# Optimization experiments

Measured on AMD Instinct MI355X. Metric: run time of the kernel, lower is better.

## Reference

```python
import jax, jax.numpy as jnp
import numpy as np

INP = 768      # inp_dim
HID = 768      # head_dim * head_num
H = 8          # head_num
D = 96         # head_dim
UP = 1536      # p_factor * inp_dim
KER = 4        # causal conv kernel size
CAP = 15.0     # gate_soft_cap
EPS = 1e-6
FUSED_OUT = 2 * H + 4 * HID  # 3088: i(8) f(8) o(768) q(768) k(768) v(768)


def _ln(x, g, b):
    mu = jnp.mean(x, axis=-1, keepdims=True)
    var = jnp.mean(jnp.square(x - mu), axis=-1, keepdims=True)
    return (x - mu) * jax.lax.rsqrt(var + EPS) * g + b


def setup_inputs() -> dict:
    key = jax.random.key(0)
    ks = jax.random.split(key, 8)
    s = 0.02
    return {
        "x": jax.random.normal(ks[0], (8, 1024, INP), dtype=jnp.float32),
        "ln1_g": jnp.ones((INP,), jnp.float32),
        "ln1_b": jnp.zeros((INP,), jnp.float32),
        "W_up_l": jax.random.normal(ks[1], (UP, INP), jnp.float32) * s,
        "W_up_r": jax.random.normal(ks[2], (HID, INP), jnp.float32) * s,
        "conv_w": jax.random.normal(ks[3], (KER,), jnp.float32) * 0.5,
        "W_skip": jax.random.normal(ks[4], (HID, UP), jnp.float32) * s,
        "fused_W": jax.random.normal(ks[5], (FUSED_OUT, UP), jnp.float32) * s,
        "fused_b": jnp.zeros((FUSED_OUT,), jnp.float32),
        "ln2_g": jnp.ones((HID,), jnp.float32),
        "ln2_b": jnp.zeros((HID,), jnp.float32),
        "W_down": jax.random.normal(ks[6], (INP, HID), jnp.float32) * s,
    }


def reference(x, ln1_g, ln1_b, W_up_l, W_up_r, conv_w, W_skip,
              fused_W, fused_b, ln2_g, ln2_b, W_down):
    B, S, _ = x.shape
    inv_sqrt_d = 1.0 / np.sqrt(D).astype(np.float32)

    def step(carry, x_row):           # x_row: [B, INP]
        C, n, m = carry               # [B,H,D,D], [B,H,D], [B,H]
        x_n = _ln(x_row, ln1_g, ln1_b)
        xt = x_n @ W_up_l.T           # [B, UP]
        rt = x_n @ W_up_r.T           # [B, HID]
        # causal conv over feature axis (left pad ker-1, 4-tap correlation)
        xp = jnp.pad(xt, ((0, 0), (KER - 1, 0)))
        xc = conv_w[0] * xp[:, 0:UP] + conv_w[1] * xp[:, 1:1 + UP] \
           + conv_w[2] * xp[:, 2:2 + UP] + conv_w[3] * xp[:, 3:3 + UP]
        xc = jax.nn.silu(xc)
        x_skip = xc @ W_skip.T        # [B, HID]
        fused = xc @ fused_W.T + fused_b  # [B, 3088]
        i_t = CAP * jnp.tanh(fused[:, :H] / CAP)                   # [B,H]
        f_t = CAP * jnp.tanh(fused[:, H:2 * H] / CAP)              # [B,H]
        # NOTE: original soft-caps o_gate too ('gate' in name) before sigmoid
        o_t = jax.nn.sigmoid(CAP * jnp.tanh(fused[:, 2 * H:2 * H + HID] / CAP))
        q = fused[:, 2 * H + HID:2 * H + 2 * HID].reshape(B, H, D)
        k = fused[:, 2 * H + 2 * HID:2 * H + 3 * HID].reshape(B, H, D) * inv_sqrt_d
        v = fused[:, 2 * H + 3 * HID:].reshape(B, H, D)
        m_t = jnp.maximum(f_t + m, i_t)
        ie = jnp.exp(i_t - m_t)
        fe = jnp.exp(f_t - m_t + m)
        C_t = fe[:, :, None, None] * C + ie[:, :, None, None] * jnp.einsum('bhd,bhe->bhde', v, k)
        n_t = fe[:, :, None] * n + ie[:, :, None] * k
        h_num = jnp.einsum('bhde,bhe->bhd', C_t, q)
        h_den = jnp.maximum(jnp.sum(n_t * q, axis=-1, keepdims=True), 1.0)
        h = o_t * (h_num / h_den).reshape(B, HID)
        out = _ln(h, ln2_g, ln2_b) @ W_down.T + x_skip
        out = out * jax.nn.silu(rt)
        return (C_t, n_t, m_t), out + x_row

    C0 = jnp.zeros((B, H, D, D), x.dtype)
    n0 = jnp.ones((B, H, D), x.dtype)
    m0 = jnp.zeros((B, H), x.dtype)
    (Cf, nf, mf), ys = jax.lax.scan(step, (C0, n0, m0), jnp.swapaxes(x, 0, 1))
    return jnp.swapaxes(ys, 0, 1), Cf, nf, mf
```

## Files before the change

### kernel.cpp

```cpp
#include <hip/hip_runtime.h>
#include <hip/hip_bf16.h>

#define NH 8
#define NB 8
#define NS 1024
#define NTOK (NB*NS)
#define CAPV 15.0f
#define EPSV 1e-6f
#define NPAD_UP 2304
#define SFW3 3968
#define OQKV_W 3072
#define INV_SQRT_D 0.10206207261596575f
#define YS_ELEMS ((size_t)NTOK * 768)
#define CH 64
#define NCH 16

typedef __attribute__((ext_vector_type(8))) short short8;
typedef __attribute__((ext_vector_type(4))) float f32x4;
typedef __hip_bfloat16 bf16;

__device__ inline float cvt(float v) { return v; }
__device__ inline float cvt(bf16 v) { return __bfloat162float(v); }

__device__ __forceinline__ void gll16(const void* g, void* l) {
  __builtin_amdgcn_global_load_lds(
      (const __attribute__((address_space(1))) void*)g,
      (__attribute__((address_space(3))) void*)l, 16, 0, 0);
}

__global__ void cast_pad_kernel(const float* __restrict__ src, bf16* __restrict__ dst, long n) {
  long i = (long)blockIdx.x * 256 + threadIdx.x;
  if (i < n) dst[i] = __float2bfloat16(src[i]);
}

__global__ void build_wsf2_kernel(const float* __restrict__ Wskip, const float* __restrict__ fusedW,
                                  bf16* __restrict__ dst) {
  int k = blockIdx.x * 256 + threadIdx.x;
  int r = blockIdx.y;
  float v;
  if (r < 768) v = Wskip[(size_t)r * 1536 + k];
  else if (r < 784) v = fusedW[(size_t)(r - 768) * 1536 + k];
  else if (r < 832) v = 0.f;
  else if (r < 3904) v = fusedW[(size_t)(r - 816) * 1536 + k];
  else v = 0.f;
  dst[(size_t)r * 1536 + k] = __float2bfloat16(v);
}

__global__ void build_bias2_kernel(const float* __restrict__ fb, float* __restrict__ bias) {
  int i = blockIdx.x * 256 + threadIdx.x;
  if (i >= SFW3) return;
  float v = 0.f;
  if (i >= 768 && i < 784) v = fb[i - 768];
  else if (i >= 832 && i < 3904) v = fb[i - 816];
  bias[i] = v;
}

template <typename T>
__global__ __launch_bounds__(256) void ln_kernel(const T* __restrict__ x,
    const float* __restrict__ g, const float* __restrict__ bta, bf16* __restrict__ out) {
  int row = blockIdx.x;
  const T* xr = x + (size_t)row * 768;
  int t = threadIdx.x;
  float v0 = cvt(xr[t]), v1 = cvt(xr[t + 256]), v2 = cvt(xr[t + 512]);
  float ssum = v0 + v1 + v2;
  __shared__ float red[8];
  #pragma unroll
  for (int m = 1; m < 64; m <<= 1) ssum += __shfl_xor(ssum, m);
  int wave = t >> 6, lane = t & 63;
  if (lane == 0) red[wave] = ssum;
  __syncthreads();
  float mu = (red[0] + red[1] + red[2] + red[3]) * (1.0f / 768.0f);
  float d0 = v0 - mu, d1 = v1 - mu, d2 = v2 - mu;
  float sq = d0 * d0 + d1 * d1 + d2 * d2;
  #pragma unroll
  for (int m = 1; m < 64; m <<= 1) sq += __shfl_xor(sq, m);
  if (lane == 0) red[wave + 4] = sq;
  __syncthreads();
  float var = (red[4] + red[5] + red[6] + red[7]) * (1.0f / 768.0f);
  float rs = rsqrtf(var + EPSV);
  size_t o = (size_t)row * 768;
  out[o + t]       = __float2bfloat16(d0 * rs * g[t]       + bta[t]);
  out[o + t + 256] = __float2bfloat16(d1 * rs * g[t + 256] + bta[t + 256]);
  out[o + t + 512] = __float2bfloat16(d2 * rs * g[t + 512] + bta[t + 512]);
}

__device__ __forceinline__ void gemm128_core(
    const bf16* __restrict__ A, const bf16* __restrict__ W, int K,
    bf16* Als, bf16* Bls, f32x4 (&acc)[4][4]) {
  int tid = threadIdx.x;
  int lane = tid & 63, wv = tid >> 6;
  int wr = wv >> 1, wc = wv & 1;
  int n0 = blockIdx.x * 128, m0 = blockIdx.y * 128;
  int rsel = lane & 15, kg = lane >> 4;
  const bf16* gA0 = A + (size_t)(m0 + lane) * K + wv * 8;
  const bf16* gA1 = A + (size_t)(m0 + 64 + lane) * K + wv * 8;
  const bf16* gB0 = W + (size_t)(n0 + lane) * K + wv * 8;
  const bf16* gB1 = W + (size_t)(n0 + 64 + lane) * K + wv * 8;
  char* lA = (char*)Als + wv * 2048;
  char* lB = (char*)Bls + wv * 2048;
  const short8* rA = (const short8*)((char*)Als + kg * 2048 + (wr * 64 + rsel) * 16);
  const short8* rB = (const short8*)((char*)Bls + kg * 2048 + (wc * 64 + rsel) * 16);
  #pragma unroll
  for (int i = 0; i < 4; i++)
    #pragma unroll
    for (int j = 0; j < 4; j++) acc[i][j] = (f32x4){0.f, 0.f, 0.f, 0.f};
  for (int k0 = 0; k0 < K; k0 += 32) {
    gll16(gA0 + k0, lA);
    gll16(gA1 + k0, lA + 1024);
    gll16(gB0 + k0, lB);
    gll16(gB1 + k0, lB + 1024);
    __syncthreads();
    short8 af[4], bw[4];
    #pragma unroll
    for (int i = 0; i < 4; i++) af[i] = rA[i * 16];
    #pragma unroll
    for (int j = 0; j < 4; j++) bw[j] = rB[j * 16];
    #pragma unroll
    for (int i = 0; i < 4; i++)
      #pragma unroll
      for (int j = 0; j < 4; j++)
        acc[i][j] = __builtin_amdgcn_mfma_f32_16x16x32_bf16(af[i], bw[j], acc[i][j], 0, 0, 0);
    __syncthreads();
  }
}

#define EPI_BASES                                              \
  int lane = threadIdx.x & 63, wv = threadIdx.x >> 6;          \
  int crow_base = blockIdx.y * 128 + (wv >> 1) * 64 + (lane >> 4) * 4; \
  int ccol_base = blockIdx.x * 128 + (wv & 1) * 64 + (lane & 15);

__global__ __launch_bounds__(256) void gemm_up_kernel(const bf16* __restrict__ A,
    const bf16* __restrict__ W, bf16* __restrict__ C, int N, int K) {
  __shared__ bf16 Als[4096], Bls[4096];
  f32x4 acc[4][4];
  gemm128_core(A, W, K, Als, Bls, acc);
  EPI_BASES
  #pragma unroll
  for (int i = 0; i < 4; i++)
    #pragma unroll
    for (int j = 0; j < 4; j++) {
      int col = ccol_base + j * 16;
      #pragma unroll
      for (int r = 0; r < 4; r++)
        C[(size_t)(crow_base + i * 16 + r) * N + col] = __float2bfloat16(acc[i][j][r]);
    }
}

__global__ __launch_bounds__(256) void gemm_sf_kernel(const bf16* __restrict__ A,
    const bf16* __restrict__ W, const float* __restrict__ bias,
    bf16* __restrict__ skipb, float* __restrict__ gates, bf16* __restrict__ oqkv) {
  __shared__ bf16 Als[4096], Bls[4096];
  f32x4 acc[4][4];
  gemm128_core(A, W, 1536, Als, Bls, acc);
  EPI_BASES
  #pragma unroll
  for (int i = 0; i < 4; i++)
    #pragma unroll
    for (int j = 0; j < 4; j++) {
      int col = ccol_base + j * 16;
      float bv = bias[col];
      #pragma unroll
      for (int r = 0; r < 4; r++) {
        int row = crow_base + i * 16 + r;
        float v = acc[i][j][r] + bv;
        if (col < 768)        skipb[(size_t)row * 768 + col] = __float2bfloat16(v);
        else if (col < 832)   gates[(size_t)row * 64 + (col - 768)] = v;
        else if (col < 3904)  oqkv[(size_t)row * OQKV_W + (col - 832)] = __float2bfloat16(v);
      }
    }
}

__global__ __launch_bounds__(256) void gemm_down_kernel(const bf16* __restrict__ A,
    const bf16* __restrict__ W, const bf16* __restrict__ skipb, const bf16* __restrict__ srt,
    const float* __restrict__ x, float* __restrict__ ys) {
  __shared__ bf16 Als[4096], Bls[4096];
  f32x4 acc[4][4];
  gemm128_core(A, W, 768, Als, Bls, acc);
  EPI_BASES
  #pragma unroll
  for (int i = 0; i < 4; i++)
    #pragma unroll
    for (int j = 0; j < 4; j++) {
      int col = ccol_base + j * 16;
      #pragma unroll
      for (int r = 0; r < 4; r++) {
        size_t idx = (size_t)(crow_base + i * 16 + r) * 768 + col;
        ys[idx] = (acc[i][j][r] + cvt(skipb[idx])) * cvt(srt[idx]) + x[idx];
      }
    }
}

__global__ __launch_bounds__(256) void conv_silu_kernel(const bf16* __restrict__ up,
    const float* __restrict__ cw, bf16* __restrict__ xc, bf16* __restrict__ srt) {
  int row = blockIdx.x;
  const bf16* xr = up + (size_t)row * NPAD_UP;
  float w0 = cw[0], w1 = cw[1], w2 = cw[2], w3 = cw[3];
  int t = threadIdx.x;
  #pragma unroll
  for (int u = 0; u < 6; ++u) {
    int j = t + u * 256;
    float xm3 = j >= 3 ? cvt(xr[j - 3]) : 0.f;
    float xm2 = j >= 2 ? cvt(xr[j - 2]) : 0.f;
    float xm1 = j >= 1 ? cvt(xr[j - 1]) : 0.f;
    float x0  = cvt(xr[j]);
    float c = w0 * xm3 + w1 * xm2 + w2 * xm1 + w3 * x0;
    xc[(size_t)row * 1536 + j] = __float2bfloat16(c / (1.f + expf(-c)));
  }
  #pragma unroll
  for (int u = 0; u < 3; ++u) {
    int j = t + u * 256;
    float r = cvt(xr[1536 + j]);
    srt[(size_t)row * 768 + j] = __float2bfloat16(r / (1.f + expf(-r)));
  }
}

__global__ __launch_bounds__(256) void gate_cap_kernel(const float* __restrict__ gates,
    float* __restrict__ icapT, float* __restrict__ fcapT) {
  int idx = blockIdx.x * 256 + threadIdx.x;
  int bh = idx >> 10, t = idx & 1023;
  int b = bh >> 3, h = bh & 7;
  size_t row = (size_t)(b * 1024 + t) * 64;
  icapT[idx] = CAPV * tanhf(gates[row + h] * (1.f / CAPV));
  fcapT[idx] = CAPV * tanhf(gates[row + 8 + h] * (1.f / CAPV));
}

__global__ __launch_bounds__(64) void mscan_kernel(const float* __restrict__ icapT,
    const float* __restrict__ fcapT, float* __restrict__ mbuf, float* __restrict__ Abuf,
    float* __restrict__ mf) {
  int bh = threadIdx.x;
  int base = bh * 1024;
  float m = 0.f, A = 0.f;
  for (int t0 = 0; t0 < 1024; t0 += 4) {
    f32x4 fc = *reinterpret_cast<const f32x4*>(fcapT + base + t0);
    f32x4 ic = *reinterpret_cast<const f32x4*>(icapT + base + t0);
    f32x4 mo, Ao;
    #pragma unroll
    for (int u = 0; u < 4; ++u) {
      A = (((t0 + u) & (CH - 1)) == 0) ? fc[u] : A + fc[u];
      m = fmaxf(fc[u] + m, ic[u]);
      mo[u] = m; Ao[u] = A;
    }
    *reinterpret_cast<f32x4*>(mbuf + base + t0) = mo;
    *reinterpret_cast<f32x4*>(Abuf + base + t0) = Ao;
  }
  mf[bh] = m;
}

__global__ __launch_bounds__(256) void chunk_kernel(
    const bf16* __restrict__ oqkv, const float* __restrict__ icapT,
    const float* __restrict__ mbuf, const float* __restrict__ Abuf,
    bf16* __restrict__ hbuf, bf16* __restrict__ UC, float* __restrict__ nUn,
    float* __restrict__ denp) {
  int bh = blockIdx.x, c = blockIdx.y;
  int b = bh >> 3, h = bh & 7;
  int tid = threadIdx.x, lane = tid & 63, wv = tid >> 6;
  int mh = wv >> 1, nh = wv & 1;
  int rsel = lane & 15, koff = (lane >> 4) * 8;
  int crow = (lane >> 4) * 4, ccol = lane & 15;
  __shared__ float At[CH], mt[CH], colt[CH], wsh[CH], rsw[2][CH];
  __shared__ bf16 P[CH][72];
  __shared__ bf16 Vt[96][72];
  __shared__ bf16 Kw[96][72];
  int t0g = c * CH;
  size_t grow0 = (size_t)(b * 1024 + t0g);
  const int qcol = 768 + h * 96, kcol = 1536 + h * 96, vcol = 2304 + h * 96;
  if (tid < CH) {
    float a  = Abuf[bh * 1024 + t0g + tid];
    float mm = mbuf[bh * 1024 + t0g + tid];
    float ic = icapT[bh * 1024 + t0g + tid];
    At[tid] = a; mt[tid] = mm; colt[tid] = ic - a;
  }
  __syncthreads();
  if (tid < CH) wsh[tid] = INV_SQRT_D * expf((At[CH - 1] - mt[CH - 1]) + colt[tid]);
  __syncthreads();
  #pragma unroll
  for (int it = 0; it < (CH * 96) / 256; ++it) {
    int idx = tid + it * 256;
    int s = idx / 96, e = idx - s * 96;
    const bf16* rp = oqkv + (grow0 + s) * OQKV_W;
    Vt[e][s] = rp[vcol + e];
    Kw[e][s] = __float2bfloat16(wsh[s] * cvt(rp[kcol + e]));
  }
  {
    const bf16* aptr = oqkv + (grow0 + mh * 32 + rsel) * OQKV_W + qcol + koff;
    const bf16* wptr = oqkv + (grow0 + nh * 32 + rsel) * OQKV_W + kcol + koff;
    f32x4 sacc[2][2];
    #pragma unroll
    for (int i = 0; i < 2; i++)
      #pragma unroll
      for (int j = 0; j < 2; j++) sacc[i][j] = (f32x4){0.f, 0.f, 0.f, 0.f};
    for (int k0 = 0; k0 < 96; k0 += 32) {
      short8 af[2], bfr[2];
      #pragma unroll
      for (int i = 0; i < 2; i++)
        af[i] = *reinterpret_cast<const short8*>(aptr + (size_t)i * 16 * OQKV_W + k0);
      #pragma unroll
      for (int j = 0; j < 2; j++)
        bfr[j] = *reinterpret_cast<const short8*>(wptr + (size_t)j * 16 * OQKV_W + k0);
      #pragma unroll
      for (int i = 0; i < 2; i++)
        #pragma unroll
        for (int j = 0; j < 2; j++)
          sacc[i][j] = __builtin_amdgcn_mfma_f32_16x16x32_bf16(af[i], bfr[j], sacc[i][j], 0, 0, 0);
    }
    float rsum[2][4] = {};
    #pragma unroll
    for (int i = 0; i < 2; i++)
      #pragma unroll
      for (int j = 0; j < 2; j++) {
        int col = nh * 32 + ccol + j * 16;
        #pragma unroll
        for (int r = 0; r < 4; r++) {
          int row = mh * 32 + crow + i * 16 + r;
          float v = 0.f;
          if (col <= row)
            v = sacc[i][j][r] * (INV_SQRT_D * expf((At[row] - mt[row]) + colt[col]));
          P[row][col] = __float2bfloat16(v);
          rsum[i][r] += v;
        }
      }
    #pragma unroll
    for (int msk = 1; msk < 16; msk <<= 1)
      #pragma unroll
      for (int i = 0; i < 2; i++)
        #pragma unroll
        for (int r = 0; r < 4; r++) rsum[i][r] += __shfl_xor(rsum[i][r], msk);
    if (ccol == 0)
      #pragma unroll
      for (int i = 0; i < 2; i++)
        #pragma unroll
        for (int r = 0; r < 4; r++) rsw[nh][mh * 32 + crow + i * 16 + r] = rsum[i][r];
  }
  __syncthreads();
  if (tid < CH) denp[bh * 1024 + t0g + tid] = rsw[0][tid] + rsw[1][tid];
  {
    f32x4 pacc[2][3];
    #pragma unroll
    for (int i = 0; i < 2; i++)
      #pragma unroll
      for (int j = 0; j < 3; j++) pacc[i][j] = (f32x4){0.f, 0.f, 0.f, 0.f};
    const bf16* pp = &P[mh * 32 + rsel][0];
    for (int k0 = 0; k0 < CH; k0 += 32) {
      short8 af[2], bfr[3];
      #pragma unroll
      for (int i = 0; i < 2; i++)
        af[i] = *reinterpret_cast<const short8*>(pp + (size_t)i * 16 * 72 + koff + k0);
      #pragma unroll
      for (int j = 0; j < 3; j++)
        bfr[j] = *reinterpret_cast<const short8*>(&Vt[nh * 48 + j * 16 + rsel][0] + koff + k0);
      #pragma unroll
      for (int i = 0; i < 2; i++)
        #pragma unroll
        for (int j = 0; j < 3; j++)
          pacc[i][j] = __builtin_amdgcn_mfma_f32_16x16x32_bf16(af[i], bfr[j], pacc[i][j], 0, 0, 0);
    }
    #pragma unroll
    for (int i = 0; i < 2; i++)
      #pragma unroll
      for (int j = 0; j < 3; j++) {
        int col = nh * 48 + ccol + j * 16;
        #pragma unroll
        for (int r = 0; r < 4; r++) {
          int row = mh * 32 + crow + i * 16 + r;
          hbuf[(grow0 + row) * 768 + h * 96 + col] = __float2bfloat16(pacc[i][j][r]);
        }
      }
  }
  {
    f32x4 uacc[3][3];
    #pragma unroll
    for (int i = 0; i < 3; i++)
      #pragma unroll
      for (int j = 0; j < 3; j++) uacc[i][j] = (f32x4){0.f, 0.f, 0.f, 0.f};
    for (int k0 = 0; k0 < CH; k0 += 32) {
      short8 af[3], bfr[3];
      #pragma unroll
      for (int i = 0; i < 3; i++)
        af[i] = *reinterpret_cast<const short8*>(&Vt[mh * 48 + i * 16 + rsel][0] + koff + k0);
      #pragma unroll
      for (int j = 0; j < 3; j++)
        bfr[j] = *reinterpret_cast<const short8*>(&Kw[nh * 48 + j * 16 + rsel][0] + koff + k0);
      #pragma unroll
      for (int i = 0; i < 3; i++)
        #pragma unroll
        for (int j = 0; j < 3; j++)
          uacc[i][j] = __builtin_amdgcn_mfma_f32_16x16x32_bf16(af[i], bfr[j], uacc[i][j], 0, 0, 0);
    }
    size_t ub = ((size_t)c * 64 + bh) * 9216;
    #pragma unroll
    for (int i = 0; i < 3; i++)
      #pragma unroll
      for (int j = 0; j < 3; j++) {
        int e = nh * 48 + ccol + j * 16;
        #pragma unroll
        for (int r = 0; r < 4; r++) {
          int d = mh * 48 + crow + i * 16 + r;
          UC[ub + (size_t)d * 96 + e] = __float2bfloat16(uacc[i][j][r]);
        }
      }
  }
  if (tid < 96) {
    float s = 0.f;
    #pragma unroll 16
    for (int s2 = 0; s2 < CH; ++s2) s += cvt(Kw[tid][s2]);
    nUn[((size_t)c * 64 + bh) * 96 + tid] = s;
  }
}

__global__ __launch_bounds__(256) void cscan_kernel(bf16* __restrict__ UC,
    const float* __restrict__ mbuf, const float* __restrict__ Abuf, float* __restrict__ Cf) {
  int bh = blockIdx.y;
  int elem = blockIdx.x * 256 + threadIdx.x;
  if (elem >= 9216) return;
  float cur = 0.f;
  for (int c = 0; c < NCH; ++c) {
    size_t o = ((size_t)c * 64 + bh) * 9216 + elem;
    float u = cvt(UC[o]);
    UC[o] = __float2bfloat16(cur);
    float mprev = c ? mbuf[bh * 1024 + c * CH - 1] : 0.f;
    float mend  = mbuf[bh * 1024 + c * CH + CH - 1];
    float aend  = Abuf[bh * 1024 + c * CH + CH - 1];
    cur = expf(aend + mprev - mend) * cur + u;
  }
  Cf[(size_t)bh * 9216 + elem] = cur;
}

__global__ __launch_bounds__(128) void nscan_kernel(float* __restrict__ nUn,
    const float* __restrict__ mbuf, const float* __restrict__ Abuf, float* __restrict__ nf) {
  int bh = blockIdx.x, e = threadIdx.x;
  if (e >= 96) return;
  float cur = 1.f;
  for (int c = 0; c < NCH; ++c) {
    size_t o = ((size_t)c * 64 + bh) * 96 + e;
    float u = nUn[o];
    nUn[o] = cur;
    float mprev = c ? mbuf[bh * 1024 + c * CH - 1] : 0.f;
    float mend  = mbuf[bh * 1024 + c * CH + CH - 1];
    float aend  = Abuf[bh * 1024 + c * CH + CH - 1];
    cur = expf(aend + mprev - mend) * cur + u;
  }
  nf[bh * 96 + e] = cur;
}

__global__ __launch_bounds__(256) void carry_kernel(
    const bf16* __restrict__ oqkv, const bf16* __restrict__ Cst, const float* __restrict__ nstg,
    const float* __restrict__ mbuf, const float* __restrict__ Abuf,
    const float* __restrict__ denp, bf16* __restrict__ hbuf) {
  int bh = blockIdx.x, c = blockIdx.y;
  int b = bh >> 3, h = bh & 7;
  int tid = threadIdx.x, lane = tid & 63, wv = tid >> 6;
  int mh = wv >> 1, nh = wv & 1;
  int rsel = lane & 15, koff = (lane >> 4) * 8;
  int crow = (lane >> 4) * 4, ccol = lane & 15;
  __shared__ float carry[CH], den[CH], nsh[96];
  __shared__ bf16 osd[CH][104], hp[CH][104];
  int t0g = c * CH;
  size_t grow0 = (size_t)(b * 1024 + t0g);
  float mprev = c ? mbuf[bh * 1024 + t0g - 1] : 0.f;
  if (tid < 96) nsh[tid] = nstg[((size_t)c * 64 + bh) * 96 + tid];
  if (tid < CH)
    carry[tid] = expf(Abuf[bh * 1024 + t0g + tid] + mprev - mbuf[bh * 1024 + t0g + tid]);
  #pragma unroll
  for (int it = 0; it < (CH * 96) / 256; ++it) {
    int idx = tid + it * 256;
    int s = idx / 96, e = idx - s * 96;
    osd[s][e] = oqkv[(grow0 + s) * OQKV_W + h * 96 + e];
    hp[s][e]  = hbuf[(grow0 + s) * 768 + h * 96 + e];
  }
  __syncthreads();
  if (tid < CH) {
    const bf16* qr = oqkv + (grow0 + tid) * OQKV_W + 768 + h * 96;
    float qn = 0.f;
    #pragma unroll 16
    for (int e = 0; e < 96; ++e) qn += cvt(qr[e]) * nsh[e];
    den[tid] = fmaxf(denp[bh * 1024 + t0g + tid] + carry[tid] * qn, 1.f);
  }
  size_t cb = ((size_t)c * 64 + bh) * 9216;
  const bf16* aptr = oqkv + (grow0 + mh * 32 + rsel) * OQKV_W + 768 + h * 96 + koff;
  f32x4 qa[2][3];
  #pragma unroll
  for (int i = 0; i < 2; i++)
    #pragma unroll
    for (int j = 0; j < 3; j++) qa[i][j] = (f32x4){0.f, 0.f, 0.f, 0.f};
  for (int k0 = 0; k0 < 96; k0 += 32) {
    short8 af[2], bfr[3];
    #pragma unroll
    for (int i = 0; i < 2; i++)
      af[i] = *reinterpret_cast<const short8*>(aptr + (size_t)i * 16 * OQKV_W + k0);
    #pragma unroll
    for (int j = 0; j < 3; j++)
      bfr[j] = *reinterpret_cast<const short8*>(Cst + cb + (size_t)(nh * 48 + j * 16 + rsel) * 96 + koff + k0);
    #pragma unroll
    for (int i = 0; i < 2; i++)
      #pragma unroll
      for (int j = 0; j < 3; j++)
        qa[i][j] = __builtin_amdgcn_mfma_f32_16x16x32_bf16(af[i], bfr[j], qa[i][j], 0, 0, 0);
  }
  __syncthreads();
  #pragma unroll
  for (int i = 0; i < 2; i++)
    #pragma unroll
    for (int j = 0; j < 3; j++) {
      int col = nh * 48 + ccol + j * 16;
      #pragma unroll
      for (int r = 0; r < 4; r++) {
        int row = mh * 32 + crow + i * 16 + r;
        float oc = CAPV * tanhf(cvt(osd[row][col]) * (1.f / CAPV));
        float og = 1.f / (1.f + expf(-oc));
        float hv = og * (cvt(hp[row][col]) + carry[row] * qa[i][j][r]) / den[row];
        hbuf[(grow0 + row) * 768 + h * 96 + col] = __float2bfloat16(hv);
      }
    }
}

extern "C" void kernel_launch(void* const* d_in, const int* in_sizes, int n_in,
                              void* d_out, int out_size, void* d_ws, size_t ws_size,
                              hipStream_t stream) {
  const float* x       = (const float*)d_in[0];
  const float* ln1_g   = (const float*)d_in[1];
  const float* ln1_b   = (const float*)d_in[2];
  const float* W_up_l  = (const float*)d_in[3];
  const float* W_up_r  = (const float*)d_in[4];
  const float* conv_w  = (const float*)d_in[5];
  const float* W_skip  = (const float*)d_in[6];
  const float* fused_W = (const float*)d_in[7];
  const float* fused_b = (const float*)d_in[8];
  const float* ln2_g   = (const float*)d_in[9];
  const float* ln2_b   = (const float*)d_in[10];
  const float* W_down  = (const float*)d_in[11];

  char* ws = (char*)d_ws;
  size_t off = 0;
  auto carve = [&](size_t bytes) -> char* {
    char* p = ws + off;
    off += (bytes + 255) & ~(size_t)255;
    return p;
  };
  bf16* wup    = (bf16*)carve((size_t)NPAD_UP * 768 * 2);
  bf16* wsf2   = (bf16*)carve((size_t)SFW3 * 1536 * 2);
  bf16* wdn    = (bf16*)carve((size_t)768 * 768 * 2);
  float* bias2 = (float*)carve(SFW3 * 4);
  bf16* srt    = (bf16*)carve((size_t)NTOK * 768 * 2);
  bf16* skipb  = (bf16*)carve((size_t)NTOK * 768 * 2);
  float* gates = (float*)carve((size_t)NTOK * 64 * 4);
  bf16* oqkv   = (bf16*)carve((size_t)NTOK * OQKV_W * 2);
  char* xcr    = carve((size_t)NTOK * 1536 * 2);
  char* R      = carve((size_t)NTOK * 768 * 2 + (size_t)NTOK * NPAD_UP * 2);
  bf16* xn     = (bf16*)R;
  bf16* up_out = (bf16*)(R + (size_t)NTOK * 768 * 2);
  bf16* hbuf   = (bf16*)R;
  bf16* hn     = (bf16*)(R + (size_t)NTOK * 768 * 2);

  bf16* xc = (bf16*)xcr;
  size_t o2 = 0;
  auto carve2 = [&](size_t bytes) -> char* {
    char* p = xcr + o2;
    o2 += (bytes + 255) & ~(size_t)255;
    return p;
  };
  float* icapT = (float*)carve2((size_t)65536 * 4);
  float* fcapT = (float*)carve2((size_t)65536 * 4);
  float* mbuf  = (float*)carve2((size_t)65536 * 4);
  float* Abuf  = (float*)carve2((size_t)65536 * 4);
  float* denp  = (float*)carve2((size_t)65536 * 4);
  bf16*  UC    = (bf16*)carve2((size_t)NCH * 64 * 9216 * 2);
  float* nUn   = (float*)carve2((size_t)NCH * 64 * 96 * 4);

  auto blocks = [](long n) { return (unsigned)((n + 255) / 256); };

  long n1 = 1536L * 768, n2 = 768L * 768;
  cast_pad_kernel<<<blocks(n1), 256, 0, stream>>>(W_up_l, wup, n1);
  cast_pad_kernel<<<blocks(n2), 256, 0, stream>>>(W_up_r, wup + n1, n2);
  build_wsf2_kernel<<<dim3(6, SFW3), 256, 0, stream>>>(W_skip, fused_W, wsf2);
  cast_pad_kernel<<<blocks(n2), 256, 0, stream>>>(W_down, wdn, n2);
  build_bias2_kernel<<<blocks(SFW3), 256, 0, stream>>>(fused_b, bias2);

  float* out_f = (float*)d_out;
  float* Cf_out = out_f + YS_ELEMS;
  float* nf_out = Cf_out + (size_t)64 * 9216;
  float* mf_out = nf_out + 64 * 96;

  ln_kernel<float><<<NTOK, 256, 0, stream>>>(x, ln1_g, ln1_b, xn);
  gemm_up_kernel<<<dim3(NPAD_UP / 128, NTOK / 128), 256, 0, stream>>>(
      xn, wup, up_out, NPAD_UP, 768);
  conv_silu_kernel<<<NTOK, 256, 0, stream>>>(up_out, conv_w, xc, srt);
  gemm_sf_kernel<<<dim3(SFW3 / 128, NTOK / 128), 256, 0, stream>>>(
      xc, wsf2, bias2, skipb, gates, oqkv);

  gate_cap_kernel<<<256, 256, 0, stream>>>(gates, icapT, fcapT);
  mscan_kernel<<<1, 64, 0, stream>>>(icapT, fcapT, mbuf, Abuf, mf_out);
  chunk_kernel<<<dim3(64, NCH), 256, 0, stream>>>(
      oqkv, icapT, mbuf, Abuf, hbuf, UC, nUn, denp);
  cscan_kernel<<<dim3(36, 64), 256, 0, stream>>>(UC, mbuf, Abuf, Cf_out);
  nscan_kernel<<<64, 128, 0, stream>>>(nUn, mbuf, Abuf, nf_out);
  carry_kernel<<<dim3(64, NCH), 256, 0, stream>>>(
      oqkv, UC, nUn, mbuf, Abuf, denp, hbuf);

  ln_kernel<bf16><<<NTOK, 256, 0, stream>>>(hbuf, ln2_g, ln2_b, hn);
  gemm_down_kernel<<<dim3(768 / 128, NTOK / 128), 256, 0, stream>>>(
      hn, wdn, skipb, srt, x, out_f);
}
```

Measured before the change: 591.7 us.

## Double-buffer GEMM LDS loads, remap grid per XCD, fuse gate capping into epilogue

The shared 128x128 GEMM core now double-buffers its LDS tiles. It issues the global-to-LDS loads for the next K step before computing the current one, waits with explicit vmcnt counts, and uses raw barriers instead of two full syncthreads per step. All three GEMMs also remap block indices so that blocks landing on the same XCD share row tiles, which is meant to improve L2 reuse. The gate soft-cap tanh and the transpose into icapT/fcapT move into the gemm_sf epilogue, which removes the separate gate_cap kernel and the intermediate gates buffer. The costs are doubled LDS use per block and hand-written waitcnt logic that depends on how the loads are ordered.

```diff
diff --git a/kernel.cpp b/kernel.cpp
--- a/kernel.cpp
+++ b/kernel.cpp
@@ -28,6 +28,13 @@
       (__attribute__((address_space(3))) void*)l, 16, 0, 0);
 }
 
+__device__ __forceinline__ void remap_grid(int& m0, int& n0) {
+  int b = blockIdx.y * gridDim.x + blockIdx.x;
+  int xcd = b & 7, slot = b >> 3;
+  m0 = (xcd * 8 + (slot & 7)) * 128;
+  n0 = (slot >> 3) * 128;
+}
+
 __global__ void cast_pad_kernel(const float* __restrict__ src, bf16* __restrict__ dst, long n) {
   long i = (long)blockIdx.x * 256 + threadIdx.x;
   if (i < n) dst[i] = __float2bfloat16(src[i]);
@@ -86,55 +93,71 @@
 
 __device__ __forceinline__ void gemm128_core(
     const bf16* __restrict__ A, const bf16* __restrict__ W, int K,
-    bf16* Als, bf16* Bls, f32x4 (&acc)[4][4]) {
+    bf16* Als, bf16* Bls, f32x4 (&acc)[4][4], int m0, int n0) {
   int tid = threadIdx.x;
   int lane = tid & 63, wv = tid >> 6;
   int wr = wv >> 1, wc = wv & 1;
-  int n0 = blockIdx.x * 128, m0 = blockIdx.y * 128;
   int rsel = lane & 15, kg = lane >> 4;
   const bf16* gA0 = A + (size_t)(m0 + lane) * K + wv * 8;
   const bf16* gA1 = A + (size_t)(m0 + 64 + lane) * K + wv * 8;
   const bf16* gB0 = W + (size_t)(n0 + lane) * K + wv * 8;
   const bf16* gB1 = W + (size_t)(n0 + 64 + lane) * K + wv * 8;
-  char* lA = (char*)Als + wv * 2048;
-  char* lB = (char*)Bls + wv * 2048;
-  const short8* rA = (const short8*)((char*)Als + kg * 2048 + (wr * 64 + rsel) * 16);
-  const short8* rB = (const short8*)((char*)Bls + kg * 2048 + (wc * 64 + rsel) * 16);
+  char* lAb = (char*)Als + wv * 2048;
+  char* lBb = (char*)Bls + wv * 2048;
+  const char* rAb = (char*)Als + kg * 2048 + (wr * 64 + rsel) * 16;
+  const char* rBb = (char*)Bls + kg * 2048 + (wc * 64 + rsel) * 16;
   #pragma unroll
   for (int i = 0; i < 4; i++)
     #pragma unroll
     for (int j = 0; j < 4; j++) acc[i][j] = (f32x4){0.f, 0.f, 0.f, 0.f};
-  for (int k0 = 0; k0 < K; k0 += 32) {
-    gll16(gA0 + k0, lA);
-    gll16(gA1 + k0, lA + 1024);
-    gll16(gB0 + k0, lB);
-    gll16(gB1 + k0, lB + 1024);
-    __syncthreads();
+  int NK = K >> 5;
+  gll16(gA0, lAb);
+  gll16(gA1, lAb + 1024);
+  gll16(gB0, lBb);
+  gll16(gB1, lBb + 1024);
+  for (int k = 0; k < NK; ++k) {
+    int cur = (k & 1) * 8192;
+    if (k + 1 < NK) {
+      int nxt = ((k + 1) & 1) * 8192;
+      int k0 = (k + 1) << 5;
+      gll16(gA0 + k0, lAb + nxt);
+      gll16(gA1 + k0, lAb + nxt + 1024);
+      gll16(gB0 + k0, lBb + nxt);
+      gll16(gB1 + k0, lBb + nxt + 1024);
+      asm volatile("s_waitcnt vmcnt(4)" ::: "memory");
+    } else {
+      asm volatile("s_waitcnt vmcnt(0)" ::: "memory");
+    }
+    __builtin_amdgcn_s_barrier();
+    asm volatile("" ::: "memory");
     short8 af[4], bw[4];
     #pragma unroll
-    for (int i = 0; i < 4; i++) af[i] = rA[i * 16];
-    #pragma unroll
-    for (int j = 0; j < 4; j++) bw[j] = rB[j * 16];
+    for (int i = 0; i < 4; i++) af[i] = *(const short8*)(rAb + cur + i * 256);
+    #pragma unroll
+    for (int j = 0; j < 4; j++) bw[j] = *(const short8*)(rBb + cur + j * 256);
     #pragma unroll
     for (int i = 0; i < 4; i++)
       #pragma unroll
       for (int j = 0; j < 4; j++)
         acc[i][j] = __builtin_amdgcn_mfma_f32_16x16x32_bf16(af[i], bw[j], acc[i][j], 0, 0, 0);
-    __syncthreads();
-  }
-}
-
-#define EPI_BASES                                              \
+    asm volatile("" ::: "memory");
+    __builtin_amdgcn_s_barrier();
+  }
+}
+
+#define EPI_BASES(m0, n0)                                      \
   int lane = threadIdx.x & 63, wv = threadIdx.x >> 6;          \
-  int crow_base = blockIdx.y * 128 + (wv >> 1) * 64 + (lane >> 4) * 4; \
-  int ccol_base = blockIdx.x * 128 + (wv & 1) * 64 + (lane & 15);
+  int crow_base = (m0) + (wv >> 1) * 64 + (lane >> 4) * 4;     \
+  int ccol_base = (n0) + (wv & 1) * 64 + (lane & 15);
 
 __global__ __launch_bounds__(256) void gemm_up_kernel(const bf16* __restrict__ A,
     const bf16* __restrict__ W, bf16* __restrict__ C, int N, int K) {
-  __shared__ bf16 Als[4096], Bls[4096];
+  __shared__ bf16 Als[8192], Bls[8192];
   f32x4 acc[4][4];
-  gemm128_core(A, W, K, Als, Bls, acc);
-  EPI_BASES
+  int m0, n0;
+  remap_grid(m0, n0);
+  gemm128_core(A, W, K, Als, Bls, acc, m0, n0);
+  EPI_BASES(m0, n0)
   #pragma unroll
   for (int i = 0; i < 4; i++)
     #pragma unroll
@@ -148,11 +171,14 @@
 
 __global__ __launch_bounds__(256) void gemm_sf_kernel(const bf16* __restrict__ A,
     const bf16* __restrict__ W, const float* __restrict__ bias,
-    bf16* __restrict__ skipb, float* __restrict__ gates, bf16* __restrict__ oqkv) {
-  __shared__ bf16 Als[4096], Bls[4096];
+    bf16* __restrict__ skipb, float* __restrict__ icapT, float* __restrict__ fcapT,
+    bf16* __restrict__ oqkv) {
+  __shared__ bf16 Als[8192], Bls[8192];
   f32x4 acc[4][4];
-  gemm128_core(A, W, 1536, Als, Bls, acc);
-  EPI_BASES
+  int m0, n0;
+  remap_grid(m0, n0);
+  gemm128_core(A, W, 1536, Als, Bls, acc, m0, n0);
+  EPI_BASES(m0, n0)
   #pragma unroll
   for (int i = 0; i < 4; i++)
     #pragma unroll
@@ -163,9 +189,19 @@
       for (int r = 0; r < 4; r++) {
         int row = crow_base + i * 16 + r;
         float v = acc[i][j][r] + bv;
-        if (col < 768)        skipb[(size_t)row * 768 + col] = __float2bfloat16(v);
-        else if (col < 832)   gates[(size_t)row * 64 + (col - 768)] = v;
-        else if (col < 3904)  oqkv[(size_t)row * OQKV_W + (col - 832)] = __float2bfloat16(v);
+        if (col < 768) {
+          skipb[(size_t)row * 768 + col] = __float2bfloat16(v);
+        } else if (col < 832) {
+          if (col < 784) {
+            int g = col - 768;
+            float cap = CAPV * tanhf(v * (1.f / CAPV));
+            int b = row >> 10, t = row & 1023;
+            int idx = (((b << 3) | (g & 7)) << 10) | t;
+            if (g < 8) icapT[idx] = cap; else fcapT[idx] = cap;
+          }
+        } else if (col < 3904) {
+          oqkv[(size_t)row * OQKV_W + (col - 832)] = __float2bfloat16(v);
+        }
       }
     }
 }
@@ -173,10 +209,12 @@
 __global__ __launch_bounds__(256) void gemm_down_kernel(const bf16* __restrict__ A,
     const bf16* __restrict__ W, const bf16* __restrict__ skipb, const bf16* __restrict__ srt,
     const float* __restrict__ x, float* __restrict__ ys) {
-  __shared__ bf16 Als[4096], Bls[4096];
+  __shared__ bf16 Als[8192], Bls[8192];
   f32x4 acc[4][4];
-  gemm128_core(A, W, 768, Als, Bls, acc);
-  EPI_BASES
+  int m0, n0;
+  remap_grid(m0, n0);
+  gemm128_core(A, W, 768, Als, Bls, acc, m0, n0);
+  EPI_BASES(m0, n0)
   #pragma unroll
   for (int i = 0; i < 4; i++)
     #pragma unroll
@@ -212,16 +250,6 @@
     float r = cvt(xr[1536 + j]);
     srt[(size_t)row * 768 + j] = __float2bfloat16(r / (1.f + expf(-r)));
   }
-}
-
-__global__ __launch_bounds__(256) void gate_cap_kernel(const float* __restrict__ gates,
-    float* __restrict__ icapT, float* __restrict__ fcapT) {
-  int idx = blockIdx.x * 256 + threadIdx.x;
-  int bh = idx >> 10, t = idx & 1023;
-  int b = bh >> 3, h = bh & 7;
-  size_t row = (size_t)(b * 1024 + t) * 64;
-  icapT[idx] = CAPV * tanhf(gates[row + h] * (1.f / CAPV));
-  fcapT[idx] = CAPV * tanhf(gates[row + 8 + h] * (1.f / CAPV));
 }
 
 __global__ __launch_bounds__(64) void mscan_kernel(const float* __restrict__ icapT,
@@ -542,7 +570,8 @@
   float* bias2 = (float*)carve(SFW3 * 4);
   bf16* srt    = (bf16*)carve((size_t)NTOK * 768 * 2);
   bf16* skipb  = (bf16*)carve((size_t)NTOK * 768 * 2);
-  float* gates = (float*)carve((size_t)NTOK * 64 * 4);
+  float* icapT = (float*)carve((size_t)65536 * 4);
+  float* fcapT = (float*)carve((size_t)65536 * 4);
   bf16* oqkv   = (bf16*)carve((size_t)NTOK * OQKV_W * 2);
   char* xcr    = carve((size_t)NTOK * 1536 * 2);
   char* R      = carve((size_t)NTOK * 768 * 2 + (size_t)NTOK * NPAD_UP * 2);
@@ -558,8 +587,6 @@
     o2 += (bytes + 255) & ~(size_t)255;
     return p;
   };
-  float* icapT = (float*)carve2((size_t)65536 * 4);
-  float* fcapT = (float*)carve2((size_t)65536 * 4);
   float* mbuf  = (float*)carve2((size_t)65536 * 4);
   float* Abuf  = (float*)carve2((size_t)65536 * 4);
   float* denp  = (float*)carve2((size_t)65536 * 4);
@@ -585,9 +612,8 @@
       xn, wup, up_out, NPAD_UP, 768);
   conv_silu_kernel<<<NTOK, 256, 0, stream>>>(up_out, conv_w, xc, srt);
   gemm_sf_kernel<<<dim3(SFW3 / 128, NTOK / 128), 256, 0, stream>>>(
-      xc, wsf2, bias2, skipb, gates, oqkv);
-
-  gate_cap_kernel<<<256, 256, 0, stream>>>(gates, icapT, fcapT);
+      xc, wsf2, bias2, skipb, icapT, fcapT, oqkv);
+
   mscan_kernel<<<1, 64, 0, stream>>>(icapT, fcapT, mbuf, Abuf, mf_out);
   chunk_kernel<<<dim3(64, NCH), 256, 0, stream>>>(
       oqkv, icapT, mbuf, Abuf, hbuf, UC, nUn, denp);
```

Measured after the change: 575.5 us. 1.03x faster.
